# Performance work log

Measured on AMD Instinct MI355X. Metric: run time of the kernel, lower is better.

The kernel has to match this reference:

```python
import jax, jax.numpy as jnp
import numpy as np

L, H, D, V, TMAX = 6, 16, 1024, 32000, 2048
HD = D // H
EPS = 1e-5


def _ln(x, g, b):
    m = jnp.mean(x, axis=-1, keepdims=True)
    v = jnp.var(x, axis=-1, keepdims=True)
    return (x - m) * jax.lax.rsqrt(v + EPS) * g + b


def setup_inputs() -> dict:
    key = jax.random.key(0)
    ks = jax.random.split(key, 16)
    s = 0.02
    inp = {
        'idx': jax.random.randint(ks[0], (2, TMAX), 0, V),
        'targets': jax.random.randint(ks[1], (2, TMAX), 0, V),
        'tok_emb': jax.random.normal(ks[2], (V, D), jnp.float32) * s,
        'pos_emb': jax.random.normal(ks[3], (TMAX, D), jnp.float32) * s,
        'wq': jax.random.normal(ks[4], (L, D, D), jnp.float32) * s,
        'wk': jax.random.normal(ks[5], (L, D, D), jnp.float32) * s,
        'wv': jax.random.normal(ks[6], (L, D, D), jnp.float32) * s,
        'w_proj': jax.random.normal(ks[7], (L, D, D), jnp.float32) * s,
        'b_proj': jnp.zeros((L, D), jnp.float32),
        'w_fc1': jax.random.normal(ks[8], (L, D, 4 * D), jnp.float32) * s,
        'b_fc1': jnp.zeros((L, 4 * D), jnp.float32),
        'w_fc2': jax.random.normal(ks[9], (L, 4 * D, D), jnp.float32) * s,
        'b_fc2': jnp.zeros((L, D), jnp.float32),
        'ln1_g': jnp.ones((L, D), jnp.float32), 'ln1_b': jnp.zeros((L, D), jnp.float32),
        'ln2_g': jnp.ones((L, D), jnp.float32), 'ln2_b': jnp.zeros((L, D), jnp.float32),
        'lnf_g': jnp.ones((D,), jnp.float32), 'lnf_b': jnp.zeros((D,), jnp.float32),
        'w_head': jax.random.normal(ks[10], (D, V), jnp.float32) * s,
        'b_head': jnp.zeros((V,), jnp.float32),
    }
    return inp


def reference(idx, targets, tok_emb, pos_emb, wq, wk, wv, w_proj, b_proj,
              w_fc1, b_fc1, w_fc2, b_fc2, ln1_g, ln1_b, ln2_g, ln2_b,
              lnf_g, lnf_b, w_head, b_head):
    B, T = idx.shape
    x = tok_emb[idx] + pos_emb[:T]  # [B,T,D]
    causal = jnp.tril(jnp.ones((T, T), bool))
    scale = HD ** -0.5
    for l in range(L):
        h = _ln(x, ln1_g[l], ln1_b[l])
        q = (h @ wq[l]).reshape(B, T, H, HD)
        k = (h @ wk[l]).reshape(B, T, H, HD)
        v = (h @ wv[l]).reshape(B, T, H, HD)
        att = jnp.einsum('bqhd,bkhd->bhqk', q, k) * scale
        att = jnp.where(causal, att, -jnp.inf)
        att = jax.nn.softmax(att, axis=-1)  # dropout is identity in eval
        o = jnp.einsum('bhqk,bkhd->bqhd', att, v).reshape(B, T, D)
        x = x + o @ w_proj[l] + b_proj[l]
        h = _ln(x, ln2_g[l], ln2_b[l])
        x = x + jax.nn.relu(h @ w_fc1[l] + b_fc1[l]) @ w_fc2[l] + b_fc2[l]
    x = _ln(x, lnf_g, lnf_b)
    logits = x @ w_head + b_head  # [B,T,V]
    logp = jax.nn.log_softmax(logits, axis=-1)
    nll = -jnp.take_along_axis(logp, targets[..., None], axis=-1)[..., 0]
    loss = jnp.mean(nll)
    return logits, loss
```

## Files before the change

kernel.cpp:

```cpp
#include <hip/hip_runtime.h>

#define LAYERS 6
#define NH 16
#define DIM 1024
#define VOCAB 32000
#define SEQ 2048
#define NBATCH 2
#define HEADD 64
#define NROW (NBATCH*SEQ)
#define FF 4096
#define QKVS 3072
#define NCB (VOCAB/256)
#define LN_EPS 1e-5f

typedef unsigned short bfu;
typedef __attribute__((ext_vector_type(8))) short s16x8;
typedef __attribute__((ext_vector_type(4))) float f32x4;

__device__ __forceinline__ float bf2f(bfu u) { return __uint_as_float(((unsigned)u) << 16); }
__device__ __forceinline__ bfu f2bf(float x) {
  unsigned u = __float_as_uint(x);
  return (bfu)((u + 0x7fffu + ((u >> 16) & 1u)) >> 16);
}

__device__ __forceinline__ void gload16(const void* g, void* l) {
  __builtin_amdgcn_global_load_lds((const __attribute__((address_space(1))) void*)g,
                                   (__attribute__((address_space(3))) void*)l, 16, 0, 0);
}

__device__ __forceinline__ f32x4 mfma32(s16x8 a, s16x8 b, f32x4 c) {
  return __builtin_amdgcn_mfma_f32_16x16x32_bf16(a, b, c, 0, 0, 0);
}

__global__ __launch_bounds__(256) void tkernel(const float* __restrict__ in,
                                               bfu* __restrict__ out, int R, int C) {
  __shared__ bfu tile[32][33];
  int tx = threadIdx.x, ty = threadIdx.y;
  int bx = blockIdx.x * 32, by = blockIdx.y * 32;
#pragma unroll
  for (int i = 0; i < 4; ++i)
    tile[ty + i * 8][tx] = f2bf(in[(size_t)(by + ty + i * 8) * C + bx + tx]);
  __syncthreads();
#pragma unroll
  for (int i = 0; i < 4; ++i)
    out[(size_t)(bx + ty + i * 8) * R + by + tx] = tile[tx][ty + i * 8];
}

__global__ __launch_bounds__(256) void wtrans_kernel(const float* __restrict__ wq,
                                                     const float* __restrict__ wk,
                                                     const float* __restrict__ wv,
                                                     const float* __restrict__ wp,
                                                     const float* __restrict__ w1,
                                                     const float* __restrict__ w2,
                                                     bfu* __restrict__ qkvT,
                                                     bfu* __restrict__ wpT,
                                                     bfu* __restrict__ f1T,
                                                     bfu* __restrict__ f2T) {
  __shared__ bfu tile[32][33];
  int bi = blockIdx.x;
  const float* in; bfu* out; int R, C, id;
  if (bi < 4096) {
    int p = bi >> 10; id = bi & 1023;
    in = p == 0 ? wq : p == 1 ? wk : p == 2 ? wv : wp;
    out = (p == 3) ? wpT : qkvT + (size_t)p * DIM * DIM;
    R = DIM; C = DIM;
  } else if (bi < 8192) {
    id = bi - 4096; in = w1; out = f1T; R = DIM; C = FF;
  } else {
    id = bi - 8192; in = w2; out = f2T; R = FF; C = DIM;
  }
  int nbx = C >> 5;
  int bx = (id % nbx) * 32, by = (id / nbx) * 32;
  int tx = threadIdx.x, ty = threadIdx.y;
#pragma unroll
  for (int i = 0; i < 4; ++i)
    tile[ty + i * 8][tx] = f2bf(in[(size_t)(by + ty + i * 8) * C + bx + tx]);
  __syncthreads();
#pragma unroll
  for (int i = 0; i < 4; ++i)
    out[(size_t)(bx + ty + i * 8) * R + by + tx] = tile[tx][ty + i * 8];
}

__global__ __launch_bounds__(256) void vtrans_kernel(const bfu* __restrict__ qkvb,
                                                     bfu* __restrict__ vT) {
  __shared__ bfu tile[32][33];
  int bh = blockIdx.z;
  int b = bh >> 4, h = bh & 15;
  int t0 = blockIdx.x * 32, d0 = blockIdx.y * 32;
  int tx = threadIdx.x, ty = threadIdx.y;
  const bfu* in = qkvb + (size_t)b * SEQ * QKVS + 2048 + h * HEADD;
#pragma unroll
  for (int i = 0; i < 4; ++i)
    tile[ty + i * 8][tx] = in[(size_t)(t0 + ty + i * 8) * QKVS + d0 + tx];
  __syncthreads();
  bfu* out = vT + ((size_t)bh * HEADD) * SEQ;
#pragma unroll
  for (int i = 0; i < 4; ++i)
    out[(size_t)(d0 + ty + i * 8) * SEQ + t0 + tx] = tile[tx][ty + i * 8];
}

__global__ __launch_bounds__(256) void embed_kernel(const int* __restrict__ idx,
                                                    const float* __restrict__ tok,
                                                    const float* __restrict__ pos,
                                                    float* __restrict__ xf) {
  int row = blockIdx.x;
  int t = row % SEQ;
  int tokid = idx[row];
  int d0 = threadIdx.x * 4;
  float4 tv = *(const float4*)&tok[(size_t)tokid * DIM + d0];
  float4 pv = *(const float4*)&pos[(size_t)t * DIM + d0];
  float4 r;
  r.x = tv.x + pv.x; r.y = tv.y + pv.y; r.z = tv.z + pv.z; r.w = tv.w + pv.w;
  *(float4*)&xf[(size_t)row * DIM + d0] = r;
}

__global__ __launch_bounds__(256) void ln_kernel(const float* __restrict__ xf,
                                                 const float* __restrict__ gw,
                                                 const float* __restrict__ bw,
                                                 bfu* __restrict__ h) {
  int row = blockIdx.x, tid = threadIdx.x;
  const float* xr = xf + (size_t)row * DIM;
  float4 xv4 = ((const float4*)xr)[tid];
  float xv[4] = {xv4.x, xv4.y, xv4.z, xv4.w};
  float s = xv[0] + xv[1] + xv[2] + xv[3];
  float ss = xv[0]*xv[0] + xv[1]*xv[1] + xv[2]*xv[2] + xv[3]*xv[3];
  for (int o = 32; o; o >>= 1) { s += __shfl_xor(s, o); ss += __shfl_xor(ss, o); }
  __shared__ float red[8];
  int wave = tid >> 6;
  if ((tid & 63) == 0) { red[wave * 2] = s; red[wave * 2 + 1] = ss; }
  __syncthreads();
  s  = red[0] + red[2] + red[4] + red[6];
  ss = red[1] + red[3] + red[5] + red[7];
  float mean = s * (1.0f / DIM);
  float var = ss * (1.0f / DIM) - mean * mean;
  float inv = rsqrtf(var + LN_EPS);
  int i0 = tid * 4;
  float4 gv = ((const float4*)gw)[tid];
  float4 bv = ((const float4*)bw)[tid];
  ushort4 hv;
  hv.x = f2bf((xv[0] - mean) * inv * gv.x + bv.x);
  hv.y = f2bf((xv[1] - mean) * inv * gv.y + bv.y);
  hv.z = f2bf((xv[2] - mean) * inv * gv.z + bv.z);
  hv.w = f2bf((xv[3] - mean) * inv * gv.w + bv.w);
  *(ushort4*)(h + (size_t)row * DIM + i0) = hv;
}

template <int MODE>
__global__ __launch_bounds__(256) void gemm_bt(const bfu* __restrict__ A,
                                               const bfu* __restrict__ Bt,
                                               const float* __restrict__ bias,
                                               const float* resid,
                                               void* outp,
                                               int M, int N, int K) {
  __shared__ __align__(16) char sm[32768];
  const int tid = threadIdx.x;
  const int lane = tid & 63, wave = tid >> 6;
  const int c = lane & 15, g = lane >> 4;

  const int gx = gridDim.x, gy = gridDim.y;
  int orig = blockIdx.y * gx + blockIdx.x;
  int cpx = (gx * gy) >> 3;
  int swz = (orig & 7) * cpx + (orig >> 3);
  int by = swz / gx, bx = swz - by * gx;

  const int m0 = by * 128, n0 = bx * 128;
  const int wm = (wave & 1) * 64, wn = (wave >> 1) * 64;
  f32x4 acc[4][4] = {};
  const char* Ac = (const char*)A;
  const char* Bc = (const char*)Bt;
  const size_t stride = (size_t)K * 2;

  const int g1 = tid, g2 = tid + 256;
  const int r1 = g1 >> 2, j1 = g1 & 3;
  const int r2 = g2 >> 2, j2 = g2 & 3;
  const size_t a1 = (size_t)(m0 + r1) * stride + j1 * 16;
  const size_t a2 = (size_t)(m0 + r2) * stride + j2 * 16;
  const size_t b1 = (size_t)(n0 + r1) * stride + j1 * 16;
  const size_t b2 = (size_t)(n0 + r2) * stride + j2 * 16;

  auto STAGE = [&](int kt, int buf) {
    char* base = sm + buf * 16384;
    size_t ko = (size_t)kt * 64;
    gload16(Ac + a1 + ko, base + g1 * 16);
    gload16(Ac + a2 + ko, base + g2 * 16);
    gload16(Bc + b1 + ko, base + 8192 + g1 * 16);
    gload16(Bc + b2 + ko, base + 8192 + g2 * 16);
  };

  const int NT = K >> 5;
  STAGE(0, 0);
  STAGE(1, 1);
  asm volatile("s_waitcnt vmcnt(4)" ::: "memory");
  __builtin_amdgcn_s_barrier();
  __builtin_amdgcn_sched_barrier(0);

  for (int i = 0; i < NT; ++i) {
    const char* base = sm + (i & 1) * 16384;
    s16x8 af[4], bfr[4];
#pragma unroll
    for (int mi = 0; mi < 4; ++mi)
      af[mi] = *(const s16x8*)(base + (wm + mi * 16 + c) * 64 + g * 16);
#pragma unroll
    for (int ni = 0; ni < 4; ++ni)
      bfr[ni] = *(const s16x8*)(base + 8192 + (wn + ni * 16 + c) * 64 + g * 16);
    asm volatile("s_waitcnt lgkmcnt(0)" ::: "memory");
    __builtin_amdgcn_sched_barrier(0);
    __builtin_amdgcn_s_barrier();
    __builtin_amdgcn_sched_barrier(0);
    if (i + 2 < NT) STAGE(i + 2, i & 1);
    __builtin_amdgcn_s_setprio(1);
#pragma unroll
    for (int mi = 0; mi < 4; ++mi)
#pragma unroll
      for (int ni = 0; ni < 4; ++ni)
        acc[mi][ni] = mfma32(af[mi], bfr[ni], acc[mi][ni]);
    __builtin_amdgcn_s_setprio(0);
    if (i < NT - 2) {
      asm volatile("s_waitcnt vmcnt(4)" ::: "memory");
      __builtin_amdgcn_s_barrier();
      __builtin_amdgcn_sched_barrier(0);
    } else if (i == NT - 2) {
      asm volatile("s_waitcnt vmcnt(0)" ::: "memory");
      __builtin_amdgcn_s_barrier();
      __builtin_amdgcn_sched_barrier(0);
    }
  }

#pragma unroll
  for (int mi = 0; mi < 4; ++mi) {
#pragma unroll
    for (int ni = 0; ni < 4; ++ni) {
      int col = n0 + wn + ni * 16 + c;
      float bv = bias ? bias[col] : 0.0f;
#pragma unroll
      for (int jj = 0; jj < 4; ++jj) {
        int row = m0 + wm + mi * 16 + g * 4 + jj;
        float val = acc[mi][ni][jj] + bv;
        size_t oi = (size_t)row * N + col;
        if (MODE == 1) val = fmaxf(val, 0.0f);
        if (MODE == 2)      ((float*)outp)[oi] = resid[oi] + val;
        else if (MODE == 3) ((float*)outp)[oi] = val;
        else                ((bfu*)outp)[oi] = f2bf(val);
      }
    }
  }
}

template <int MODE>
__global__ __launch_bounds__(1024) void gemm1024(const bfu* __restrict__ A,
                                                 const bfu* __restrict__ Bt,
                                                 const float* __restrict__ bias,
                                                 const float* resid,
                                                 void* outp,
                                                 int M, int N, int K,
                                                 int colchunk,
                                                 float* __restrict__ pmax,
                                                 float* __restrict__ psum) {
  extern __shared__ char smem[];
  const int tid = threadIdx.x;
  const int lane = tid & 63, w = tid >> 6;
  const int c = lane & 15, g = lane >> 4;

  const int gx = gridDim.x, gy = gridDim.y;
  int orig = blockIdx.y * gx + blockIdx.x;
  int cpx = (gx * gy) >> 3;
  int swz = (orig & 7) * cpx + (orig >> 3);
  int bx, by;
  if (colchunk) { bx = swz / gy; by = swz - bx * gy; }
  else          { by = swz / gx; bx = swz - by * gx; }
  const int m0 = by * 256, n0 = bx * 256;

  const int wrow = w >> 2, wcol = w & 3;
  const size_t gstr = (size_t)K * 2;
  const char* Ag = (const char*)A + (size_t)m0 * gstr;
  const char* Bg = (const char*)Bt + (size_t)n0 * gstr;

  int srow0 = tid >> 3, scg0 = (tid & 7) ^ (srow0 & 7);
  int srow1 = (tid + 1024) >> 3, scg1 = (tid & 7) ^ (srow1 & 7);
  const size_t ga0 = (size_t)srow0 * gstr + scg0 * 16;
  const size_t ga1 = (size_t)srow1 * gstr + scg1 * 16;

  auto STAGE = [&](int kt, int buf) {
    char* base = smem + buf * 65536;
    size_t ko = (size_t)kt * 128;
    gload16(Ag + ga0 + ko, base + w * 1024);
    gload16(Ag + ga1 + ko, base + 16384 + w * 1024);
    gload16(Bg + ga0 + ko, base + 32768 + w * 1024);
    gload16(Bg + ga1 + ko, base + 49152 + w * 1024);
  };

  const int NT = K >> 6;
  f32x4 acc[4][4] = {};

  STAGE(0, 0);
  STAGE(1, 1);
  asm volatile("s_waitcnt vmcnt(4)" ::: "memory");
  __builtin_amdgcn_s_barrier();
  __builtin_amdgcn_sched_barrier(0);

  const int rsw = (c & 7) << 4;
  const int off0 = (g * 16) ^ rsw;
  const int off1 = (64 + g * 16) ^ rsw;

  for (int i = 0; i < NT; ++i) {
    const char* ldsA = smem + (i & 1) * 65536 + (wrow * 64 + c) * 128;
    const char* ldsB = smem + (i & 1) * 65536 + 32768 + (wcol * 64 + c) * 128;
    s16x8 a[4], b[4];
#pragma unroll
    for (int mi = 0; mi < 4; ++mi) a[mi] = *(const s16x8*)(ldsA + mi * 2048 + off0);
#pragma unroll
    for (int ni = 0; ni < 4; ++ni) b[ni] = *(const s16x8*)(ldsB + ni * 2048 + off0);
    __builtin_amdgcn_s_setprio(1);
#pragma unroll
    for (int mi = 0; mi < 4; ++mi)
#pragma unroll
      for (int ni = 0; ni < 4; ++ni)
        acc[mi][ni] = mfma32(a[mi], b[ni], acc[mi][ni]);
    __builtin_amdgcn_s_setprio(0);
#pragma unroll
    for (int mi = 0; mi < 4; ++mi) a[mi] = *(const s16x8*)(ldsA + mi * 2048 + off1);
#pragma unroll
    for (int ni = 0; ni < 4; ++ni) b[ni] = *(const s16x8*)(ldsB + ni * 2048 + off1);
    asm volatile("s_waitcnt lgkmcnt(0)" ::: "memory");
    __builtin_amdgcn_sched_barrier(0);
    __builtin_amdgcn_s_barrier();
    __builtin_amdgcn_sched_barrier(0);
    if (i + 2 < NT) STAGE(i + 2, i & 1);
    __builtin_amdgcn_s_setprio(1);
#pragma unroll
    for (int mi = 0; mi < 4; ++mi)
#pragma unroll
      for (int ni = 0; ni < 4; ++ni)
        acc[mi][ni] = mfma32(a[mi], b[ni], acc[mi][ni]);
    __builtin_amdgcn_s_setprio(0);
    if (i < NT - 2) {
      asm volatile("s_waitcnt vmcnt(4)" ::: "memory");
      __builtin_amdgcn_s_barrier();
      __builtin_amdgcn_sched_barrier(0);
    } else if (i == NT - 2) {
      asm volatile("s_waitcnt vmcnt(0)" ::: "memory");
      __builtin_amdgcn_s_barrier();
      __builtin_amdgcn_sched_barrier(0);
    }
  }

  if (MODE != 4) {
#pragma unroll
    for (int mi = 0; mi < 4; ++mi) {
#pragma unroll
      for (int ni = 0; ni < 4; ++ni) {
        int col = n0 + wcol * 64 + ni * 16 + c;
        float bv = bias ? bias[col] : 0.0f;
#pragma unroll
        for (int jj = 0; jj < 4; ++jj) {
          int row = m0 + wrow * 64 + mi * 16 + g * 4 + jj;
          float val = acc[mi][ni][jj] + bv;
          size_t oi = (size_t)row * N + col;
          if (MODE == 1) val = fmaxf(val, 0.0f);
          else if (MODE == 2) { ((float*)outp)[oi] = resid[oi] + val; continue; }
          if (MODE == 3) ((float*)outp)[oi] = val;
          else           ((bfu*)outp)[oi] = f2bf(val);
        }
      }
    }
  } else {
    float* sred = (float*)(smem + 131072);
    const int ncb = N >> 8;
    float bvv[4]; int colv[4];
#pragma unroll
    for (int ni = 0; ni < 4; ++ni) {
      colv[ni] = n0 + wcol * 64 + ni * 16 + c;
      bvv[ni] = bias ? bias[colv[ni]] : 0.0f;
    }
#pragma unroll
    for (int mi = 0; mi < 4; ++mi) {
#pragma unroll
      for (int jj = 0; jj < 4; ++jj) {
        int row = m0 + wrow * 64 + mi * 16 + g * 4 + jj;
        float v[4];
#pragma unroll
        for (int ni = 0; ni < 4; ++ni) {
          v[ni] = acc[mi][ni][jj] + bvv[ni];
          __builtin_nontemporal_store(v[ni], (float*)outp + (size_t)row * N + colv[ni]);
        }
        float mx = fmaxf(fmaxf(v[0], v[1]), fmaxf(v[2], v[3]));
#pragma unroll
        for (int off = 1; off < 16; off <<= 1) mx = fmaxf(mx, __shfl_xor(mx, off));
        float sm = __expf(v[0] - mx) + __expf(v[1] - mx) +
                   __expf(v[2] - mx) + __expf(v[3] - mx);
#pragma unroll
        for (int off = 1; off < 16; off <<= 1) sm += __shfl_xor(sm, off);
        if (c == 0) {
          int r64 = mi * 16 + g * 4 + jj;
          sred[(w * 64 + r64) * 2 + 0] = mx;
          sred[(w * 64 + r64) * 2 + 1] = sm;
        }
      }
    }
    __syncthreads();
    if (tid < 256) {
      int wr = tid >> 6, r64 = tid & 63;
      float M2 = -3.0e38f, S2 = 0.0f;
#pragma unroll
      for (int wc2 = 0; wc2 < 4; ++wc2) {
        float m_i = sred[((wr * 4 + wc2) * 64 + r64) * 2 + 0];
        float s_i = sred[((wr * 4 + wc2) * 64 + r64) * 2 + 1];
        float nm = fmaxf(M2, m_i);
        S2 = S2 * __expf(M2 - nm) + s_i * __expf(m_i - nm);
        M2 = nm;
      }
      size_t pi = (size_t)(m0 + tid) * ncb + bx;
      pmax[pi] = M2;
      psum[pi] = S2;
    }
  }
}

__global__ __launch_bounds__(256) void attn_kernel(const bfu* __restrict__ qkv,
                                                   const bfu* __restrict__ vT,
                                                   bfu* __restrict__ o) {
  __shared__ __align__(16) bfu Ks[64 * 64];
  __shared__ __align__(16) bfu Vt[64 * 64];
  __shared__ __align__(16) bfu Plds[4 * 16 * 32];
  const int tid = threadIdx.x;
  const int lane = tid & 63, w = tid >> 6;
  const int c = lane & 15, g = lane >> 4;
  const int qt = blockIdx.x, hh = blockIdx.y, b = blockIdx.z;
  const int q0 = qt * 64 + w * 16;
  const float SENT = -1e30f;
  const size_t rowb = (size_t)b * SEQ;

  const size_t qbase = (rowb + q0 + c) * QKVS + hh * HEADD + g * 8;
  s16x8 qf0 = *(const s16x8*)&qkv[qbase];
  s16x8 qf1 = *(const s16x8*)&qkv[qbase + 32];
  const bfu* Kg = qkv + 1024 + hh * HEADD;
  const bfu* vTb = vT + (size_t)(b * NH + hh) * HEADD * SEQ;
  bfu* Pw = Plds + w * 512;

  const int srow = tid >> 3;
  const int sgr = (tid & 7) ^ (srow & 7);
  const int cw = c & 7;

  f32x4 oacc[4] = {};
  float mrun = SENT, lrun = 0.0f;

  const int nkt = qt + 1;
  for (int kt = 0; kt < nkt; ++kt) {
    const int k0 = kt * 64;
    __syncthreads();
#pragma unroll
    for (int p = 0; p < 2; ++p) {
      int r = p * 32 + srow;
      gload16(Kg + (rowb + k0 + r) * QKVS + sgr * 8, (char*)Ks + p * 4096 + w * 1024);
      gload16(vTb + (size_t)r * SEQ + k0 + sgr * 8, (char*)Vt + p * 4096 + w * 1024);
    }
    asm volatile("s_waitcnt vmcnt(0)" ::: "memory");
    __syncthreads();

#pragma unroll
    for (int s = 0; s < 2; ++s) {
      const int k0s = k0 + s * 32;
      if (k0s <= q0 + 15) {
        const char* Kb = (const char*)Ks + (size_t)(s * 32 + c) * 128;
        s16x8 kf00 = *(const s16x8*)(Kb + ((g ^ cw) * 16));
        s16x8 kf01 = *(const s16x8*)(Kb + (((4 + g) ^ cw) * 16));
        s16x8 kf10 = *(const s16x8*)(Kb + 16 * 128 + ((g ^ cw) * 16));
        s16x8 kf11 = *(const s16x8*)(Kb + 16 * 128 + (((4 + g) ^ cw) * 16));
        f32x4 s0 = {}, s1 = {};
        s0 = mfma32(kf00, qf0, s0); s0 = mfma32(kf01, qf1, s0);
        s1 = mfma32(kf10, qf0, s1); s1 = mfma32(kf11, qf1, s1);

        float sv[8];
#pragma unroll
        for (int jj = 0; jj < 4; ++jj) {
          int ka = k0s + g * 4 + jj, kb = ka + 16;
          sv[jj]     = (ka <= q0 + c) ? s0[jj] * 0.125f : SENT;
          sv[4 + jj] = (kb <= q0 + c) ? s1[jj] * 0.125f : SENT;
        }
        float tmax = sv[0];
#pragma unroll
        for (int i = 1; i < 8; ++i) tmax = fmaxf(tmax, sv[i]);
        tmax = fmaxf(tmax, __shfl_xor(tmax, 16));
        tmax = fmaxf(tmax, __shfl_xor(tmax, 32));
        float mnew = fmaxf(mrun, tmax);
        float alpha = __expf(mrun - mnew);
        float p[8], psm = 0.0f;
#pragma unroll
        for (int i = 0; i < 8; ++i) { p[i] = __expf(sv[i] - mnew); psm += p[i]; }
        psm += __shfl_xor(psm, 16);
        psm += __shfl_xor(psm, 32);
        lrun = lrun * alpha + psm;
        mrun = mnew;

        ushort4 w0; w0.x = f2bf(p[0]); w0.y = f2bf(p[1]); w0.z = f2bf(p[2]); w0.w = f2bf(p[3]);
        ushort4 w1; w1.x = f2bf(p[4]); w1.y = f2bf(p[5]); w1.z = f2bf(p[6]); w1.w = f2bf(p[7]);
        *(ushort4*)&Pw[c * 32 + g * 4] = w0;
        *(ushort4*)&Pw[c * 32 + 16 + g * 4] = w1;
        asm volatile("s_waitcnt lgkmcnt(0)" ::: "memory");
        __builtin_amdgcn_sched_barrier(0);

        float aq[4];
#pragma unroll
        for (int jj = 0; jj < 4; ++jj) aq[jj] = __shfl(alpha, g * 4 + jj);

        ushort4 ra = *(const ushort4*)&Pw[c * 32 + g * 8];
        ushort4 rb = *(const ushort4*)&Pw[c * 32 + g * 8 + 4];
        s16x8 pa = {(short)ra.x, (short)ra.y, (short)ra.z, (short)ra.w,
                    (short)rb.x, (short)rb.y, (short)rb.z, (short)rb.w};

#pragma unroll
        for (int dg = 0; dg < 4; ++dg) {
          s16x8 vf = *(const s16x8*)((const char*)Vt + (size_t)(dg * 16 + c) * 128 +
                                     (((s * 4 + g) ^ cw) * 16));
#pragma unroll
          for (int jj = 0; jj < 4; ++jj) oacc[dg][jj] *= aq[jj];
          oacc[dg] = mfma32(pa, vf, oacc[dg]);
        }
      }
    }
  }

  float lq[4];
#pragma unroll
  for (int jj = 0; jj < 4; ++jj) lq[jj] = __shfl(lrun, g * 4 + jj);
#pragma unroll
  for (int dg = 0; dg < 4; ++dg)
#pragma unroll
    for (int jj = 0; jj < 4; ++jj) {
      size_t oi = (size_t)(rowb + q0 + g * 4 + jj) * DIM + hh * HEADD + dg * 16 + c;
      o[oi] = f2bf(oacc[dg][jj] / lq[jj]);
    }
}

__global__ __launch_bounds__(64) void nll_finish(const float* __restrict__ pmax,
                                                 const float* __restrict__ psum,
                                                 const float* __restrict__ logits,
                                                 const int* __restrict__ tgt,
                                                 float* __restrict__ nll) {
  int row = blockIdx.x, lane = threadIdx.x;
  const float* pm = pmax + (size_t)row * NCB;
  const float* ps = psum + (size_t)row * NCB;
  float m = -3.0e38f, s = 0.0f;
  if (lane < NCB) { m = pm[lane]; s = ps[lane]; }
  int i2 = lane + 64;
  if (i2 < NCB) {
    float m2 = pm[i2], s2 = ps[i2];
    float nm = fmaxf(m, m2);
    s = s * __expf(m - nm) + s2 * __expf(m2 - nm);
    m = nm;
  }
#pragma unroll
  for (int off = 32; off; off >>= 1) {
    float om = __shfl_xor(m, off), os = __shfl_xor(s, off);
    float nm = fmaxf(m, om);
    s = s * __expf(m - nm) + os * __expf(om - nm);
    m = nm;
  }
  if (lane == 0)
    nll[row] = (m + __logf(s)) - logits[(size_t)row * VOCAB + tgt[row]];
}

__global__ __launch_bounds__(256) void loss_kernel(const float* __restrict__ nll,
                                                   float* __restrict__ out) {
  float s = 0.0f;
  for (int i = threadIdx.x; i < NROW; i += 256) s += nll[i];
  for (int off = 32; off; off >>= 1) s += __shfl_xor(s, off);
  __shared__ float r[4];
  int wave = threadIdx.x >> 6;
  if ((threadIdx.x & 63) == 0) r[wave] = s;
  __syncthreads();
  if (threadIdx.x == 0) out[(size_t)NROW * VOCAB] = (r[0] + r[1] + r[2] + r[3]) * (1.0f / NROW);
}

extern "C" void kernel_launch(void* const* d_in, const int* in_sizes, int n_in,
                              void* d_out, int out_size, void* d_ws, size_t ws_size,
                              hipStream_t stream) {
  (void)in_sizes; (void)n_in; (void)out_size;
  const int* idx       = (const int*)d_in[0];
  const int* targets   = (const int*)d_in[1];
  const float* tok_emb = (const float*)d_in[2];
  const float* pos_emb = (const float*)d_in[3];
  const float* wq      = (const float*)d_in[4];
  const float* wk      = (const float*)d_in[5];
  const float* wv      = (const float*)d_in[6];
  const float* w_proj  = (const float*)d_in[7];
  const float* b_proj  = (const float*)d_in[8];
  const float* w_fc1   = (const float*)d_in[9];
  const float* b_fc1   = (const float*)d_in[10];
  const float* w_fc2   = (const float*)d_in[11];
  const float* b_fc2   = (const float*)d_in[12];
  const float* ln1_g   = (const float*)d_in[13];
  const float* ln1_b   = (const float*)d_in[14];
  const float* ln2_g   = (const float*)d_in[15];
  const float* ln2_b   = (const float*)d_in[16];
  const float* lnf_g   = (const float*)d_in[17];
  const float* lnf_b   = (const float*)d_in[18];
  const float* w_head  = (const float*)d_in[19];
  const float* b_head  = (const float*)d_in[20];

  char* ws = (char*)d_ws;
  size_t off = 0;
  auto alloc = [&](size_t bytes) {
    char* p = ws + off;
    off += (bytes + 255) & ~(size_t)255;
    return p;
  };
  float* xf   = (float*)alloc((size_t)NROW * DIM * 4);
  bfu* hbuf   = (bfu*)alloc((size_t)NROW * DIM * 2);
  bfu* qkvb   = (bfu*)alloc((size_t)NROW * QKVS * 2);
  bfu* ob     = (bfu*)alloc((size_t)NROW * DIM * 2);
  bfu* ub     = (bfu*)alloc((size_t)NROW * FF * 2);
  bfu* vT     = (bfu*)alloc((size_t)NROW * DIM * 2);
  bfu* qkvT   = (bfu*)alloc((size_t)QKVS * DIM * 2);
  bfu* wpT    = (bfu*)alloc((size_t)DIM * DIM * 2);
  bfu* f1T    = (bfu*)alloc((size_t)DIM * FF * 2);
  bfu* f2T    = (bfu*)alloc((size_t)DIM * FF * 2);
  bfu* hT     = (bfu*)alloc((size_t)DIM * VOCAB * 2);
  float* nll  = (float*)alloc((size_t)NROW * 4);
  float* pmax = (float*)alloc((size_t)NROW * NCB * 4);
  float* psum = (float*)alloc((size_t)NROW * NCB * 4);
  if (off > ws_size) return;

  const size_t LDSB = 131072;
  dim3 tb(32, 8);
  tkernel<<<dim3(VOCAB / 32, DIM / 32), tb, 0, stream>>>(w_head, hT, DIM, VOCAB);
  embed_kernel<<<NROW, 256, 0, stream>>>(idx, tok_emb, pos_emb, xf);

  float* logits = (float*)d_out;
  for (int l = 0; l < LAYERS; ++l) {
    const size_t wo = (size_t)l * DIM * DIM, fo = (size_t)l * DIM * FF;
    wtrans_kernel<<<12288, tb, 0, stream>>>(wq + wo, wk + wo, wv + wo, w_proj + wo,
                                            w_fc1 + fo, w_fc2 + fo, qkvT, wpT, f1T, f2T);
    ln_kernel<<<NROW, 256, 0, stream>>>(xf, ln1_g + l * DIM, ln1_b + l * DIM, hbuf);
    gemm_bt<0><<<dim3(QKVS / 128, NROW / 128), 256, 0, stream>>>(
        hbuf, qkvT, nullptr, nullptr, qkvb, NROW, QKVS, DIM);
    vtrans_kernel<<<dim3(SEQ / 32, HEADD / 32, NBATCH * NH), tb, 0, stream>>>(qkvb, vT);
    attn_kernel<<<dim3(SEQ / 64, NH, NBATCH), 256, 0, stream>>>(qkvb, vT, ob);
    gemm_bt<2><<<dim3(DIM / 128, NROW / 128), 256, 0, stream>>>(
        ob, wpT, b_proj + l * DIM, xf, xf, NROW, DIM, DIM);
    ln_kernel<<<NROW, 256, 0, stream>>>(xf, ln2_g + l * DIM, ln2_b + l * DIM, hbuf);
    gemm1024<1><<<dim3(FF / 256, NROW / 256), 1024, LDSB, stream>>>(
        hbuf, f1T, b_fc1 + l * FF, nullptr, ub, NROW, FF, DIM, 0, nullptr, nullptr);
    gemm_bt<2><<<dim3(DIM / 128, NROW / 128), 256, 0, stream>>>(
        ub, f2T, b_fc2 + l * DIM, xf, xf, NROW, DIM, FF);
  }

  ln_kernel<<<NROW, 256, 0, stream>>>(xf, lnf_g, lnf_b, hbuf);
  gemm1024<4><<<dim3(VOCAB / 256, NROW / 256), 1024, LDSB + 8192, stream>>>(
      hbuf, hT, b_head, nullptr, logits, NROW, VOCAB, DIM, 1, pmax, psum);
  nll_finish<<<NROW, 64, 0, stream>>>(pmax, psum, logits, targets, nll);
  loss_kernel<<<1, 256, 0, stream>>>(nll, logits);
}
```

Before: 2.300 ms.

## Use wave-per-row layernorm, lazy softmax rescale in attention, plain logits stores

Layernorm now gives one wave to each row and processes four rows per block, which removes the shared-memory reduction and the block barrier. In the attention inner loop, the running-max update and the rescaling of the output accumulator are skipped whenever every new score stays within 8 of the current max. The logits store in the head GEMM switches from a nontemporal store to a regular store. The deferred rescale lets exponentials reach up to e^8 before normalization, which in fp32 and bf16 adds a small precision risk.

```diff
diff --git a/kernel.cpp b/kernel.cpp
--- a/kernel.cpp
+++ b/kernel.cpp
@@ -118,31 +118,32 @@
                                                  const float* __restrict__ gw,
                                                  const float* __restrict__ bw,
                                                  bfu* __restrict__ h) {
-  int row = blockIdx.x, tid = threadIdx.x;
+  const int row = blockIdx.x * 4 + (threadIdx.x >> 6);
+  const int lane = threadIdx.x & 63;
   const float* xr = xf + (size_t)row * DIM;
-  float4 xv4 = ((const float4*)xr)[tid];
-  float xv[4] = {xv4.x, xv4.y, xv4.z, xv4.w};
-  float s = xv[0] + xv[1] + xv[2] + xv[3];
-  float ss = xv[0]*xv[0] + xv[1]*xv[1] + xv[2]*xv[2] + xv[3]*xv[3];
+  float4 xv[4];
+  float s = 0.0f, ss = 0.0f;
+#pragma unroll
+  for (int j = 0; j < 4; ++j) {
+    xv[j] = *(const float4*)&xr[lane * 4 + j * 256];
+    s  += xv[j].x + xv[j].y + xv[j].z + xv[j].w;
+    ss += xv[j].x * xv[j].x + xv[j].y * xv[j].y + xv[j].z * xv[j].z + xv[j].w * xv[j].w;
+  }
+#pragma unroll
   for (int o = 32; o; o >>= 1) { s += __shfl_xor(s, o); ss += __shfl_xor(ss, o); }
-  __shared__ float red[8];
-  int wave = tid >> 6;
-  if ((tid & 63) == 0) { red[wave * 2] = s; red[wave * 2 + 1] = ss; }
-  __syncthreads();
-  s  = red[0] + red[2] + red[4] + red[6];
-  ss = red[1] + red[3] + red[5] + red[7];
   float mean = s * (1.0f / DIM);
-  float var = ss * (1.0f / DIM) - mean * mean;
-  float inv = rsqrtf(var + LN_EPS);
-  int i0 = tid * 4;
-  float4 gv = ((const float4*)gw)[tid];
-  float4 bv = ((const float4*)bw)[tid];
-  ushort4 hv;
-  hv.x = f2bf((xv[0] - mean) * inv * gv.x + bv.x);
-  hv.y = f2bf((xv[1] - mean) * inv * gv.y + bv.y);
-  hv.z = f2bf((xv[2] - mean) * inv * gv.z + bv.z);
-  hv.w = f2bf((xv[3] - mean) * inv * gv.w + bv.w);
-  *(ushort4*)(h + (size_t)row * DIM + i0) = hv;
+  float inv = rsqrtf(ss * (1.0f / DIM) - mean * mean + LN_EPS);
+#pragma unroll
+  for (int j = 0; j < 4; ++j) {
+    float4 gv = *(const float4*)&gw[lane * 4 + j * 256];
+    float4 bv = *(const float4*)&bw[lane * 4 + j * 256];
+    ushort4 hv;
+    hv.x = f2bf((xv[j].x - mean) * inv * gv.x + bv.x);
+    hv.y = f2bf((xv[j].y - mean) * inv * gv.y + bv.y);
+    hv.z = f2bf((xv[j].z - mean) * inv * gv.z + bv.z);
+    hv.w = f2bf((xv[j].w - mean) * inv * gv.w + bv.w);
+    *(ushort4*)&h[(size_t)row * DIM + lane * 4 + j * 256] = hv;
+  }
 }
 
 template <int MODE>
@@ -381,7 +382,7 @@
 #pragma unroll
         for (int ni = 0; ni < 4; ++ni) {
           v[ni] = acc[mi][ni][jj] + bvv[ni];
-          __builtin_nontemporal_store(v[ni], (float*)outp + (size_t)row * N + colv[ni]);
+          ((float*)outp)[(size_t)row * N + colv[ni]] = v[ni];
         }
         float mx = fmaxf(fmaxf(v[0], v[1]), fmaxf(v[2], v[3]));
 #pragma unroll
@@ -482,15 +483,14 @@
         for (int i = 1; i < 8; ++i) tmax = fmaxf(tmax, sv[i]);
         tmax = fmaxf(tmax, __shfl_xor(tmax, 16));
         tmax = fmaxf(tmax, __shfl_xor(tmax, 32));
-        float mnew = fmaxf(mrun, tmax);
-        float alpha = __expf(mrun - mnew);
+
+        bool defer = __all(tmax <= mrun + 8.0f) && (kt | s);
+        float mref = defer ? mrun : fmaxf(mrun, tmax);
         float p[8], psm = 0.0f;
 #pragma unroll
-        for (int i = 0; i < 8; ++i) { p[i] = __expf(sv[i] - mnew); psm += p[i]; }
+        for (int i = 0; i < 8; ++i) { p[i] = __expf(sv[i] - mref); psm += p[i]; }
         psm += __shfl_xor(psm, 16);
         psm += __shfl_xor(psm, 32);
-        lrun = lrun * alpha + psm;
-        mrun = mnew;
 
         ushort4 w0; w0.x = f2bf(p[0]); w0.y = f2bf(p[1]); w0.z = f2bf(p[2]); w0.w = f2bf(p[3]);
         ushort4 w1; w1.x = f2bf(p[4]); w1.y = f2bf(p[5]); w1.z = f2bf(p[6]); w1.w = f2bf(p[7]);
@@ -499,9 +499,21 @@
         asm volatile("s_waitcnt lgkmcnt(0)" ::: "memory");
         __builtin_amdgcn_sched_barrier(0);
 
-        float aq[4];
-#pragma unroll
-        for (int jj = 0; jj < 4; ++jj) aq[jj] = __shfl(alpha, g * 4 + jj);
+        if (defer) {
+          lrun += psm;
+        } else {
+          float mnew = mref;
+          float alpha = __expf(mrun - mnew);
+          lrun = lrun * alpha + psm;
+          mrun = mnew;
+          float aq[4];
+#pragma unroll
+          for (int jj = 0; jj < 4; ++jj) aq[jj] = __shfl(alpha, g * 4 + jj);
+#pragma unroll
+          for (int dg = 0; dg < 4; ++dg)
+#pragma unroll
+            for (int jj = 0; jj < 4; ++jj) oacc[dg][jj] *= aq[jj];
+        }
 
         ushort4 ra = *(const ushort4*)&Pw[c * 32 + g * 8];
         ushort4 rb = *(const ushort4*)&Pw[c * 32 + g * 8 + 4];
@@ -512,8 +524,6 @@
         for (int dg = 0; dg < 4; ++dg) {
           s16x8 vf = *(const s16x8*)((const char*)Vt + (size_t)(dg * 16 + c) * 128 +
                                      (((s * 4 + g) ^ cw) * 16));
-#pragma unroll
-          for (int jj = 0; jj < 4; ++jj) oacc[dg][jj] *= aq[jj];
           oacc[dg] = mfma32(pa, vf, oacc[dg]);
         }
       }
@@ -631,21 +641,21 @@
     const size_t wo = (size_t)l * DIM * DIM, fo = (size_t)l * DIM * FF;
     wtrans_kernel<<<12288, tb, 0, stream>>>(wq + wo, wk + wo, wv + wo, w_proj + wo,
                                             w_fc1 + fo, w_fc2 + fo, qkvT, wpT, f1T, f2T);
-    ln_kernel<<<NROW, 256, 0, stream>>>(xf, ln1_g + l * DIM, ln1_b + l * DIM, hbuf);
+    ln_kernel<<<NROW / 4, 256, 0, stream>>>(xf, ln1_g + l * DIM, ln1_b + l * DIM, hbuf);
     gemm_bt<0><<<dim3(QKVS / 128, NROW / 128), 256, 0, stream>>>(
         hbuf, qkvT, nullptr, nullptr, qkvb, NROW, QKVS, DIM);
     vtrans_kernel<<<dim3(SEQ / 32, HEADD / 32, NBATCH * NH), tb, 0, stream>>>(qkvb, vT);
     attn_kernel<<<dim3(SEQ / 64, NH, NBATCH), 256, 0, stream>>>(qkvb, vT, ob);
     gemm_bt<2><<<dim3(DIM / 128, NROW / 128), 256, 0, stream>>>(
         ob, wpT, b_proj + l * DIM, xf, xf, NROW, DIM, DIM);
-    ln_kernel<<<NROW, 256, 0, stream>>>(xf, ln2_g + l * DIM, ln2_b + l * DIM, hbuf);
+    ln_kernel<<<NROW / 4, 256, 0, stream>>>(xf, ln2_g + l * DIM, ln2_b + l * DIM, hbuf);
     gemm1024<1><<<dim3(FF / 256, NROW / 256), 1024, LDSB, stream>>>(
         hbuf, f1T, b_fc1 + l * FF, nullptr, ub, NROW, FF, DIM, 0, nullptr, nullptr);
     gemm_bt<2><<<dim3(DIM / 128, NROW / 128), 256, 0, stream>>>(
         ub, f2T, b_fc2 + l * DIM, xf, xf, NROW, DIM, FF);
   }
 
-  ln_kernel<<<NROW, 256, 0, stream>>>(xf, lnf_g, lnf_b, hbuf);
+  ln_kernel<<<NROW / 4, 256, 0, stream>>>(xf, lnf_g, lnf_b, hbuf);
   gemm1024<4><<<dim3(VOCAB / 256, NROW / 256), 1024, LDSB + 8192, stream>>>(
       hbuf, hT, b_head, nullptr, logits, NROW, VOCAB, DIM, 1, pmax, psum);
   nll_finish<<<NROW, 64, 0, stream>>>(pmax, psum, logits, targets, nll);
```

After: 2.208 ms. 1.04x faster.
